# Optimization experiments

Hardware: AMD Instinct MI355X
Metric: run time of the kernel (lower is better)

The kernel has to match this reference:

```python
import jax, jax.numpy as jnp
import numpy as np
import math

N_HEAD = 16


def _causal_attn(q, k, v):
    # q: [B,H,L,d], k/v: [B,H,S,d]; standard scaled-dot-product causal attention
    d_k = q.shape[-1]
    s = jnp.einsum('bhqd,bhkd->bhqk', q, k) / math.sqrt(d_k)
    L, S = q.shape[-2], k.shape[-2]
    mask = jnp.tril(jnp.ones((L, S), dtype=bool))
    s = jnp.where(mask, s, -jnp.inf)
    a = jax.nn.softmax(s, axis=-1)
    return jnp.einsum('bhqk,bhkd->bhqd', a, v)


def setup_inputs() -> dict:
    key = jax.random.key(0)
    ks = jax.random.split(key, 8)
    B, T, C = 2, 2048, 1024
    scale = 0.02
    return {
        'x': jax.random.normal(ks[0], (B, T, C), dtype=jnp.float32),
        'W_attn': jax.random.normal(ks[1], (C, 2 * C), dtype=jnp.float32) * scale,
        'b_attn': jnp.zeros((2 * C,), dtype=jnp.float32),
        'W_k2': jax.random.normal(ks[2], (C, C), dtype=jnp.float32) * scale,
        'b_k2': jnp.zeros((C,), dtype=jnp.float32),
        'W_proj': jax.random.normal(ks[3], (C, C), dtype=jnp.float32) * scale,
        'b_proj': jnp.zeros((C,), dtype=jnp.float32),
    }


def reference(x, W_attn, b_attn, W_k2, b_k2, W_proj, b_proj):
    # Eval-mode forward of CausalSelfAttentionARMA (all dropouts inactive).
    B, T, C = x.shape
    H = N_HEAD
    d = C // H

    qk = x @ W_attn + b_attn                      # [B,T,2C]
    q, k = qk[..., :C], qk[..., C:]
    q = q.reshape(B, T, H, d).transpose(0, 2, 1, 3)   # [B,H,T,d]
    k = k.reshape(B, T, H, d).transpose(0, 2, 1, 3)
    v = x.reshape(B, T, H, d).transpose(0, 2, 1, 3)   # v = x (no value proj)

    # AR pass: standard causal attention
    y = _causal_attn(q, k, v)                     # [B,H,T,d]

    # MA residual: e_t = v_{t+1} - y_t
    e = v[:, :, 1:, :] - y[:, :, :-1, :]          # [B,H,T-1,d]

    k2 = (x[:, :-1] @ W_k2 + b_k2).reshape(B, T - 1, H, d).transpose(0, 2, 1, 3)
    q2 = q[:, :, 1:, :]

    # MA pass: second causal attention over residuals
    y2 = _causal_attn(q2, k2, e)                  # [B,H,T-1,d]
    y2 = jnp.concatenate([jnp.zeros_like(y2[:, :, :1, :]), y2], axis=2)  # [B,H,T,d]

    def proj(t):
        return t.transpose(0, 2, 1, 3).reshape(B, T, C) @ W_proj + b_proj

    return proj(y) + proj(y2)
```

## Files before the change

kernel.cpp:

```cpp
#include <hip/hip_runtime.h>
#include <hip/hip_bf16.h>

typedef unsigned short u16;
typedef short s16x8 __attribute__((ext_vector_type(8)));
typedef float f32x4 __attribute__((ext_vector_type(4)));
typedef float f32x16 __attribute__((ext_vector_type(16)));
typedef unsigned int u32x4 __attribute__((ext_vector_type(4)));

#define LOG2E 1.44269504088896f

__device__ __forceinline__ u16 f2b(float f){
    __hip_bfloat16 h = __float2bfloat16(f);
    return __builtin_bit_cast(unsigned short, h);
}
__device__ __forceinline__ float b2f(u16 u){
    __hip_bfloat16 h = __builtin_bit_cast(__hip_bfloat16, u);
    return __bfloat162float(h);
}
__device__ __forceinline__ unsigned int pk2(float a, float b){
    return (unsigned int)f2b(a) | ((unsigned int)f2b(b) << 16);
}

__global__ void k_f32_to_bf16(const float* __restrict__ in, u16* __restrict__ out, int n4){
    int i = blockIdx.x*blockDim.x + threadIdx.x;
    int stride = gridDim.x*blockDim.x;
    for (; i < n4; i += stride){
        float4 a = *(const float4*)&in[(size_t)i*4];
        uint2 o;
        o.x = pk2(a.x, a.y);
        o.y = pk2(a.z, a.w);
        *(uint2*)&out[(size_t)i*4] = o;
    }
}

__global__ void k_transpose_bf16(const float* __restrict__ W, u16* __restrict__ Wt, int K, int N){
    __shared__ float tile[32][33];
    int n0 = blockIdx.x*32, k0 = blockIdx.y*32;
    int c = threadIdx.x & 31, r0 = threadIdx.x >> 5;
#pragma unroll
    for (int it = 0; it < 4; ++it){
        int r = r0 + it*8;
        tile[r][c] = W[(size_t)(k0+r)*N + n0 + c];
    }
    __syncthreads();
#pragma unroll
    for (int it = 0; it < 4; ++it){
        int r = r0 + it*8;
        Wt[(size_t)(n0+r)*K + k0 + c] = f2b(tile[c][r]);
    }
}

__global__ __launch_bounds__(256) void k_build_vT(const float* __restrict__ x, u16* __restrict__ VT){
    __shared__ float tile[64][65];
    int bh = blockIdx.x, t0 = blockIdx.y*64;
    int b = bh >> 4, h = bh & 15;
    int tid = threadIdx.x;
    {
        int tt = tid >> 2, ds = (tid & 3)*16;
        const float* xp = &x[((size_t)(b*2048) + t0 + tt)*1024 + h*64 + ds];
#pragma unroll
        for (int j4 = 0; j4 < 4; ++j4){
            float4 a = *(const float4*)&xp[j4*4];
            tile[tt][ds + j4*4 + 0] = a.x;
            tile[tt][ds + j4*4 + 1] = a.y;
            tile[tt][ds + j4*4 + 2] = a.z;
            tile[tt][ds + j4*4 + 3] = a.w;
        }
    }
    __syncthreads();
    {
        int dd = tid >> 2, ts = (tid & 3)*16;
        unsigned int o[8];
#pragma unroll
        for (int j = 0; j < 8; ++j)
            o[j] = pk2(tile[ts + 2*j][dd], tile[ts + 2*j + 1][dd]);
        u16* dst = &VT[((size_t)(bh*64 + dd))*2048 + t0 + ts];
        *(uint4*)&dst[0] = *(uint4*)&o[0];
        *(uint4*)&dst[8] = *(uint4*)&o[4];
    }
}

__global__ __launch_bounds__(256) void k_compute_eT(const float* __restrict__ x, const float* __restrict__ y1T,
                                                    u16* __restrict__ ET){
    __shared__ float tile[64][65];
    int bh = blockIdx.x, j0 = blockIdx.y*64;
    int b = bh >> 4, h = bh & 15;
    int tid = threadIdx.x;
    {
        int tt = tid >> 2, ds = (tid & 3)*16;
        int j = j0 + tt;
        int xr = (j <= 2046) ? (j + 1) : 2047;
        const float* xp = &x[((size_t)(b*2048) + xr)*1024 + h*64 + ds];
#pragma unroll
        for (int j4 = 0; j4 < 4; ++j4){
            float4 a = *(const float4*)&xp[j4*4];
            tile[tt][ds + j4*4 + 0] = a.x;
            tile[tt][ds + j4*4 + 1] = a.y;
            tile[tt][ds + j4*4 + 2] = a.z;
            tile[tt][ds + j4*4 + 3] = a.w;
        }
    }
    __syncthreads();
    {
        int dd = tid >> 2, ts = (tid & 3)*16;
        const float* yp = &y1T[((size_t)(bh*64 + dd))*2048 + j0 + ts];
        unsigned int o[8];
#pragma unroll
        for (int j = 0; j < 8; ++j){
            int c0 = ts + 2*j, c1 = ts + 2*j + 1;
            float e0 = (j0 + c0 <= 2046) ? (tile[c0][dd] - yp[2*j])   : 0.f;
            float e1 = (j0 + c1 <= 2046) ? (tile[c1][dd] - yp[2*j+1]) : 0.f;
            o[j] = pk2(e0, e1);
        }
        u16* dst = &ET[((size_t)(bh*64 + dd))*2048 + j0 + ts];
        *(uint4*)&dst[0] = *(uint4*)&o[0];
        *(uint4*)&dst[8] = *(uint4*)&o[4];
    }
}

template<int MODE>
__global__ __launch_bounds__(256) void k_gemm(const u16* __restrict__ A, const u16* __restrict__ Bt,
                       const float* __restrict__ bias, float* __restrict__ outF,
                       u16* __restrict__ out0, u16* __restrict__ out1,
                       int M, int N, int K){
    __shared__ u16 As[128][72];
    __shared__ u16 Bs[128][72];
    int m0 = blockIdx.y * 128, n0 = blockIdx.x * 128;
    int tid = threadIdx.x;
    int lane = tid & 63, w = tid >> 6;
    int wm = w >> 1, wn = w & 1;
    int l15 = lane & 15, l4 = lane >> 4;
    f32x4 acc[4][4] = {};

    for (int kt = 0; kt < K; kt += 64){
#pragma unroll
        for (int it = 0; it < 4; ++it){
            int c = tid + 256*it;
            int row = c >> 3, seg = c & 7;
            *(uint4*)&As[row][seg*8] = *(const uint4*)&A[(size_t)(m0+row)*K + kt + seg*8];
            *(uint4*)&Bs[row][seg*8] = *(const uint4*)&Bt[(size_t)(n0+row)*K + kt + seg*8];
        }
        __syncthreads();
#pragma unroll
        for (int kk = 0; kk < 2; ++kk){
            s16x8 a[4], b[4];
#pragma unroll
            for (int mi = 0; mi < 4; ++mi)
                a[mi] = *(const s16x8*)&As[wm*64 + mi*16 + l15][kk*32 + l4*8];
#pragma unroll
            for (int ni = 0; ni < 4; ++ni)
                b[ni] = *(const s16x8*)&Bs[wn*64 + ni*16 + l15][kk*32 + l4*8];
#pragma unroll
            for (int mi = 0; mi < 4; ++mi)
#pragma unroll
                for (int ni = 0; ni < 4; ++ni)
                    acc[mi][ni] = __builtin_amdgcn_mfma_f32_16x16x32_bf16(a[mi], b[ni], acc[mi][ni], 0,0,0);
        }
        __syncthreads();
    }

#pragma unroll
    for (int mi = 0; mi < 4; ++mi){
        int growb = m0 + wm*64 + mi*16 + l4*4;
#pragma unroll
        for (int ni = 0; ni < 4; ++ni){
            int gcol = n0 + wn*64 + ni*16 + l15;
            float bv = bias[gcol];
#pragma unroll
            for (int r = 0; r < 4; ++r){
                int row = growb + r;
                float val = acc[mi][ni][r];
                if (MODE == 2){
                    outF[(size_t)row*N + gcol] = val + 2.0f*bv;
                } else {
                    val += bv;
                    int bb = row >> 11, t = row & 2047;
                    if (MODE == 0){
                        if (gcol < 1024){
                            int h = gcol >> 6, dd = gcol & 63;
                            out0[(((size_t)(bb*16+h))*2048 + t)*64 + dd] = f2b(val*0.125f);
                        } else {
                            int c2 = gcol - 1024;
                            int h = c2 >> 6, dd = c2 & 63;
                            out1[(((size_t)(bb*16+h))*2048 + t)*64 + dd] = f2b(val);
                        }
                    } else {
                        int h = gcol >> 6, dd = gcol & 63;
                        out0[(((size_t)(bb*16+h))*2048 + t)*64 + dd] = f2b(val);
                    }
                }
            }
        }
    }
}

__global__ __launch_bounds__(256) void k_flash32(const u16* __restrict__ Q, const u16* __restrict__ Km,
                         const u16* __restrict__ VT, float* __restrict__ OT,
                         int Tq, int Tkv, int qoff){
    __shared__ u16 Ks[64*64];
    __shared__ u16 Vs[64*64];
    int bh = blockIdx.x;
    int yy = blockIdx.y;
    int t = (yy < 8) ? yy : (15 - (yy - 8));
    int tid = threadIdx.x;
    int lane = tid & 63, w = tid >> 6;
    int l31 = lane & 31, hi = lane >> 5;
    const u16* Qp = Q + ((size_t)bh*2048 + qoff)*64;
    const u16* Kp = Km + (size_t)bh*2048*64;
    const u16* Vp = VT + (size_t)bh*64*2048;
    float* Op = OT + (size_t)bh*64*2048;

    int srow = tid >> 2;
    int sc   = tid & 3;

    int ntile = 2*t + 2;
    int q0w = t*128 + w*32;
    int qi = q0w + l31; if (qi > Tq-1) qi = Tq-1;

    s16x8 qf[4];
#pragma unroll
    for (int st = 0; st < 4; ++st)
        qf[st] = *(const s16x8*)&Qp[(size_t)qi*64 + st*16 + hi*8];

    f32x16 accO[2] = {};
    float m_r = -INFINITY, l_r = 0.f;

    uint4 kr0, kr1, vr0, vr1;
    {
        int kvr = srow; if (kvr > Tkv-1) kvr = Tkv-1;
        kr0 = *(const uint4*)&Kp[(size_t)kvr*64 + sc*16];
        kr1 = *(const uint4*)&Kp[(size_t)kvr*64 + sc*16 + 8];
        vr0 = *(const uint4*)&Vp[(size_t)srow*2048 + sc*16];
        vr1 = *(const uint4*)&Vp[(size_t)srow*2048 + sc*16 + 8];
    }

    for (int i = 0; i < ntile; ++i){
        int kv0 = i*64;
        {
            int sw = srow & 7;
            *(uint4*)&Ks[srow*64 + (((2*sc)   ^ sw)*8)] = kr0;
            *(uint4*)&Ks[srow*64 + (((2*sc+1) ^ sw)*8)] = kr1;
            *(uint4*)&Vs[srow*64 + (((2*sc)   ^ sw)*8)] = vr0;
            *(uint4*)&Vs[srow*64 + (((2*sc+1) ^ sw)*8)] = vr1;
        }
        __syncthreads();
        if (i + 1 < ntile){
            int kv1 = kv0 + 64;
            int kvr = kv1 + srow; if (kvr > Tkv-1) kvr = Tkv-1;
            kr0 = *(const uint4*)&Kp[(size_t)kvr*64 + sc*16];
            kr1 = *(const uint4*)&Kp[(size_t)kvr*64 + sc*16 + 8];
            vr0 = *(const uint4*)&Vp[(size_t)srow*2048 + kv1 + sc*16];
            vr1 = *(const uint4*)&Vp[(size_t)srow*2048 + kv1 + sc*16 + 8];
        }
        if (kv0 <= q0w + 31){
            f32x16 accS[2] = {};
            __builtin_amdgcn_s_setprio(1);
#pragma unroll
            for (int m = 0; m < 2; ++m){
                int row = 32*m + l31;
                int sw = row & 7;
#pragma unroll
                for (int st = 0; st < 4; ++st){
                    s16x8 a = *(const s16x8*)&Ks[row*64 + (((2*st + hi) ^ sw)*8)];
                    accS[m] = __builtin_amdgcn_mfma_f32_32x32x16_bf16(a, qf[st], accS[m], 0,0,0);
                }
            }
            __builtin_amdgcn_s_setprio(0);
            float p[32];
            bool diag = (kv0 + 63 > q0w);
#pragma unroll
            for (int m = 0; m < 2; ++m)
#pragma unroll
                for (int r = 0; r < 16; ++r){
                    float s = accS[m][r];
                    if (diag){
                        int kg = kv0 + 32*m + (r&3) + 8*(r>>2) + 4*hi;
                        if (kg > qi) s = -INFINITY;
                    }
                    p[m*16 + r] = s;
                }
            float mx = p[0];
#pragma unroll
            for (int j = 1; j < 32; ++j) mx = fmaxf(mx, p[j]);
            mx = fmaxf(mx, __shfl_xor(mx, 32));
            float mnew = fmaxf(m_r, mx);
            if (!__all(mx - m_r <= 8.f)){
                float scl = exp2f((m_r - mnew)*LOG2E);
#pragma unroll
                for (int dt = 0; dt < 2; ++dt)
#pragma unroll
                    for (int r = 0; r < 16; ++r) accO[dt][r] *= scl;
                l_r *= scl;
                m_r = mnew;
            }
            float rs = 0.f;
#pragma unroll
            for (int j = 0; j < 32; ++j){
                p[j] = exp2f((p[j] - m_r)*LOG2E);
                rs += p[j];
            }
            rs += __shfl_xor(rs, 32);
            l_r += rs;
#pragma unroll
            for (int m = 0; m < 2; ++m)
#pragma unroll
                for (int s2 = 0; s2 < 2; ++s2){
                    const float* pp = &p[m*16 + s2*8];
                    unsigned dwa = pk2(pp[0], pp[1]);
                    unsigned dwb = pk2(pp[2], pp[3]);
                    unsigned dwc = pk2(pp[4], pp[5]);
                    unsigned dwd = pk2(pp[6], pp[7]);
                    unsigned xa = (unsigned)__shfl_xor((int)dwa, 32);
                    unsigned xb = (unsigned)__shfl_xor((int)dwb, 32);
                    unsigned xc = (unsigned)__shfl_xor((int)dwc, 32);
                    unsigned xd = (unsigned)__shfl_xor((int)dwd, 32);
                    u32x4 fv;
                    fv.x = hi ? xc : dwa;
                    fv.y = hi ? xd : dwb;
                    fv.z = hi ? dwc : xa;
                    fv.w = hi ? dwd : xb;
                    s16x8 pf = __builtin_bit_cast(s16x8, fv);
                    int vslot = m*4 + s2*2 + hi;
                    __builtin_amdgcn_s_setprio(1);
#pragma unroll
                    for (int dt = 0; dt < 2; ++dt){
                        int vrow = dt*32 + l31;
                        s16x8 va = *(const s16x8*)&Vs[vrow*64 + ((vslot ^ (vrow&7))*8)];
                        accO[dt] = __builtin_amdgcn_mfma_f32_32x32x16_bf16(va, pf, accO[dt], 0,0,0);
                    }
                    __builtin_amdgcn_s_setprio(0);
                }
        }
        __syncthreads();
    }
    float inv = 1.0f / l_r;
#pragma unroll
    for (int dt = 0; dt < 2; ++dt)
#pragma unroll
        for (int r = 0; r < 16; ++r){
            int d = dt*32 + (r&3) + 8*(r>>2) + 4*hi;
            Op[(size_t)d*2048 + qi] = accO[dt][r] * inv;
        }
}

__global__ __launch_bounds__(256) void k_ysum(const float* __restrict__ y1T, const float* __restrict__ y2T,
                                              u16* __restrict__ ys){
    __shared__ float tile[64][65];
    int bh = blockIdx.x, t0 = blockIdx.y*64;
    int b = bh >> 4, h = bh & 15;
    int tid = threadIdx.x;
    {
        int dd = tid >> 2, ts = (tid & 3)*16;
        const float* y1p = &y1T[((size_t)(bh*64 + dd))*2048 + t0 + ts];
        const float* y2p = &y2T[((size_t)(bh*64 + dd))*2048 + t0 + ts - 1];
#pragma unroll
        for (int c = 0; c < 16; ++c){
            int tg = t0 + ts + c;
            float s = y1p[c];
            if (tg > 0) s += y2p[c];
            tile[ts + c][dd] = s;
        }
    }
    __syncthreads();
    {
        int tt = tid >> 2, ds = (tid & 3)*16;
        unsigned int o[8];
#pragma unroll
        for (int j = 0; j < 8; ++j)
            o[j] = pk2(tile[tt][ds + 2*j], tile[tt][ds + 2*j + 1]);
        u16* dst = &ys[((size_t)(b*2048) + t0 + tt)*1024 + h*64 + ds];
        *(uint4*)&dst[0] = *(uint4*)&o[0];
        *(uint4*)&dst[8] = *(uint4*)&o[4];
    }
}

extern "C" void kernel_launch(void* const* d_in, const int* in_sizes, int n_in,
                              void* d_out, int out_size, void* d_ws, size_t ws_size,
                              hipStream_t stream){
    const float* x      = (const float*)d_in[0];
    const float* W_attn = (const float*)d_in[1];
    const float* b_attn = (const float*)d_in[2];
    const float* W_k2   = (const float*)d_in[3];
    const float* b_k2   = (const float*)d_in[4];
    const float* W_proj = (const float*)d_in[5];
    const float* b_proj = (const float*)d_in[6];
    float* out = (float*)d_out;

    char* ws = (char*)d_ws;
    size_t off = 0;
    auto alloc = [&](size_t bytes)->void*{
        void* p = ws + off; off += (bytes + 255) & ~size_t(255); return p;
    };
    u16* xb    = (u16*)alloc((size_t)4096*1024*2);
    u16* WaT   = (u16*)alloc((size_t)2048*1024*2);
    u16* Wk2T  = (u16*)alloc((size_t)1024*1024*2);
    u16* WpT   = (u16*)alloc((size_t)1024*1024*2);
    u16* Qb    = (u16*)alloc((size_t)32*2048*64*2);
    u16* Kb    = (u16*)alloc((size_t)32*2048*64*2);
    u16* VTg   = (u16*)alloc((size_t)32*64*2048*2);
    u16* K2b   = (u16*)alloc((size_t)32*2048*64*2);
    u16* ETg   = (u16*)alloc((size_t)32*64*2048*2);
    float* y1T = (float*)alloc((size_t)32*64*2048*4);
    float* y2T = (float*)alloc((size_t)32*64*2048*4);
    u16* ys    = (u16*)alloc((size_t)4096*1024*2);

    k_f32_to_bf16<<<1024, 256, 0, stream>>>(x, xb, 1<<20);
    k_transpose_bf16<<<dim3(64, 32), 256, 0, stream>>>(W_attn, WaT, 1024, 2048);
    k_transpose_bf16<<<dim3(32, 32), 256, 0, stream>>>(W_k2, Wk2T, 1024, 1024);
    k_transpose_bf16<<<dim3(32, 32), 256, 0, stream>>>(W_proj, WpT, 1024, 1024);
    k_build_vT<<<dim3(32, 32), 256, 0, stream>>>(x, VTg);

    k_gemm<0><<<dim3(16, 32), 256, 0, stream>>>(xb, WaT, b_attn, nullptr, Qb, Kb, 4096, 2048, 1024);
    k_gemm<1><<<dim3(8, 32), 256, 0, stream>>>(xb, Wk2T, b_k2, nullptr, K2b, nullptr, 4096, 1024, 1024);

    k_flash32<<<dim3(32, 16), 256, 0, stream>>>(Qb, Kb, VTg, y1T, 2048, 2048, 0);
    k_compute_eT<<<dim3(32, 32), 256, 0, stream>>>(x, y1T, ETg);
    k_flash32<<<dim3(32, 16), 256, 0, stream>>>(Qb, K2b, ETg, y2T, 2047, 2047, 1);
    k_ysum<<<dim3(32, 32), 256, 0, stream>>>(y1T, y2T, ys);

    k_gemm<2><<<dim3(8, 32), 256, 0, stream>>>(ys, WpT, b_proj, out, nullptr, nullptr, 4096, 1024, 1024);
}
```

Before: 359.8 us.

## Rewrite flash attention to read K/V directly from global memory without LDS

The flash kernel no longer stages K and V tiles through shared memory with block-wide barriers. Each wave now loads its MFMA operands straight from global memory, relying on L1/L2 to serve the reuse. Blocks shrink to 128 threads with twice as many blocks, and each wave skips KV tiles past its own causal limit, so only the last tile needs masking. It also packs bf16 with the hardware cvt_pk instruction and folds the softmax scale into an fma. The trade-off is more global/cache traffic and less data reuse per block.

```diff
diff --git a/kernel.cpp b/kernel.cpp
--- a/kernel.cpp
+++ b/kernel.cpp
@@ -19,6 +19,11 @@
 }
 __device__ __forceinline__ unsigned int pk2(float a, float b){
     return (unsigned int)f2b(a) | ((unsigned int)f2b(b) << 16);
+}
+__device__ __forceinline__ unsigned int cvtpk(float lo, float hi){
+    unsigned int r;
+    asm("v_cvt_pk_bf16_f32 %0, %1, %2" : "=v"(r) : "v"(lo), "v"(hi));
+    return r;
 }
 
 __global__ void k_f32_to_bf16(const float* __restrict__ in, u16* __restrict__ out, int n4){
@@ -194,28 +199,24 @@
     }
 }
 
-__global__ __launch_bounds__(256) void k_flash32(const u16* __restrict__ Q, const u16* __restrict__ Km,
+__global__ __launch_bounds__(128) void k_flashw(const u16* __restrict__ Q, const u16* __restrict__ Km,
                          const u16* __restrict__ VT, float* __restrict__ OT,
-                         int Tq, int Tkv, int qoff){
-    __shared__ u16 Ks[64*64];
-    __shared__ u16 Vs[64*64];
+                         int Tq, int qoff){
     int bh = blockIdx.x;
-    int yy = blockIdx.y;
-    int t = (yy < 8) ? yy : (15 - (yy - 8));
+    int y = blockIdx.y;
+    int t = (y < 16) ? (15 - (y >> 1)) : ((y - 16) >> 1);
+    int half = y & 1;
     int tid = threadIdx.x;
-    int lane = tid & 63, w = tid >> 6;
+    int w = tid >> 6, lane = tid & 63;
     int l31 = lane & 31, hi = lane >> 5;
     const u16* Qp = Q + ((size_t)bh*2048 + qoff)*64;
     const u16* Kp = Km + (size_t)bh*2048*64;
     const u16* Vp = VT + (size_t)bh*64*2048;
     float* Op = OT + (size_t)bh*64*2048;
 
-    int srow = tid >> 2;
-    int sc   = tid & 3;
-
-    int ntile = 2*t + 2;
-    int q0w = t*128 + w*32;
+    int q0w = t*128 + half*64 + w*32;
     int qi = q0w + l31; if (qi > Tq-1) qi = Tq-1;
+    int nt = (q0w >> 6) + 1;
 
     s16x8 qf[4];
 #pragma unroll
@@ -225,113 +226,103 @@
     f32x16 accO[2] = {};
     float m_r = -INFINITY, l_r = 0.f;
 
-    uint4 kr0, kr1, vr0, vr1;
-    {
-        int kvr = srow; if (kvr > Tkv-1) kvr = Tkv-1;
-        kr0 = *(const uint4*)&Kp[(size_t)kvr*64 + sc*16];
-        kr1 = *(const uint4*)&Kp[(size_t)kvr*64 + sc*16 + 8];
-        vr0 = *(const uint4*)&Vp[(size_t)srow*2048 + sc*16];
-        vr1 = *(const uint4*)&Vp[(size_t)srow*2048 + sc*16 + 8];
-    }
-
-    for (int i = 0; i < ntile; ++i){
+    for (int i = 0; i < nt; ++i){
         int kv0 = i*64;
+        const u16* kb = Kp + (size_t)kv0*64;
+        f32x16 s0 = {}, s1 = {};
         {
-            int sw = srow & 7;
-            *(uint4*)&Ks[srow*64 + (((2*sc)   ^ sw)*8)] = kr0;
-            *(uint4*)&Ks[srow*64 + (((2*sc+1) ^ sw)*8)] = kr1;
-            *(uint4*)&Vs[srow*64 + (((2*sc)   ^ sw)*8)] = vr0;
-            *(uint4*)&Vs[srow*64 + (((2*sc+1) ^ sw)*8)] = vr1;
-        }
-        __syncthreads();
-        if (i + 1 < ntile){
-            int kv1 = kv0 + 64;
-            int kvr = kv1 + srow; if (kvr > Tkv-1) kvr = Tkv-1;
-            kr0 = *(const uint4*)&Kp[(size_t)kvr*64 + sc*16];
-            kr1 = *(const uint4*)&Kp[(size_t)kvr*64 + sc*16 + 8];
-            vr0 = *(const uint4*)&Vp[(size_t)srow*2048 + kv1 + sc*16];
-            vr1 = *(const uint4*)&Vp[(size_t)srow*2048 + kv1 + sc*16 + 8];
-        }
-        if (kv0 <= q0w + 31){
-            f32x16 accS[2] = {};
+            const u16* kr0 = kb + (size_t)l31*64 + hi*8;
+            const u16* kr1 = kb + (size_t)(32 + l31)*64 + hi*8;
+            s16x8 a0 = *(const s16x8*)&kr0[0];
+            s16x8 a1 = *(const s16x8*)&kr0[16];
+            s16x8 a2 = *(const s16x8*)&kr0[32];
+            s16x8 a3 = *(const s16x8*)&kr0[48];
+            s16x8 b0 = *(const s16x8*)&kr1[0];
+            s16x8 b1 = *(const s16x8*)&kr1[16];
+            s16x8 b2 = *(const s16x8*)&kr1[32];
+            s16x8 b3 = *(const s16x8*)&kr1[48];
             __builtin_amdgcn_s_setprio(1);
-#pragma unroll
-            for (int m = 0; m < 2; ++m){
-                int row = 32*m + l31;
-                int sw = row & 7;
-#pragma unroll
-                for (int st = 0; st < 4; ++st){
-                    s16x8 a = *(const s16x8*)&Ks[row*64 + (((2*st + hi) ^ sw)*8)];
-                    accS[m] = __builtin_amdgcn_mfma_f32_32x32x16_bf16(a, qf[st], accS[m], 0,0,0);
-                }
+            s0 = __builtin_amdgcn_mfma_f32_32x32x16_bf16(a0, qf[0], s0, 0,0,0);
+            s1 = __builtin_amdgcn_mfma_f32_32x32x16_bf16(b0, qf[0], s1, 0,0,0);
+            s0 = __builtin_amdgcn_mfma_f32_32x32x16_bf16(a1, qf[1], s0, 0,0,0);
+            s1 = __builtin_amdgcn_mfma_f32_32x32x16_bf16(b1, qf[1], s1, 0,0,0);
+            s0 = __builtin_amdgcn_mfma_f32_32x32x16_bf16(a2, qf[2], s0, 0,0,0);
+            s1 = __builtin_amdgcn_mfma_f32_32x32x16_bf16(b2, qf[2], s1, 0,0,0);
+            s0 = __builtin_amdgcn_mfma_f32_32x32x16_bf16(a3, qf[3], s0, 0,0,0);
+            s1 = __builtin_amdgcn_mfma_f32_32x32x16_bf16(b3, qf[3], s1, 0,0,0);
+            __builtin_amdgcn_s_setprio(0);
+        }
+        if (i == nt - 1){
+#pragma unroll
+            for (int r = 0; r < 16; ++r){
+                int kg0 = kv0 + (r&3) + 8*(r>>2) + 4*hi;
+                if (kg0 > qi) s0[r] = -INFINITY;
+                if (kg0 + 32 > qi) s1[r] = -INFINITY;
             }
+        }
+        float mx = s0[0];
+#pragma unroll
+        for (int r = 1; r < 16; ++r) mx = fmaxf(mx, s0[r]);
+#pragma unroll
+        for (int r = 0; r < 16; ++r) mx = fmaxf(mx, s1[r]);
+        mx = fmaxf(mx, __shfl_xor(mx, 32));
+        float mnew = fmaxf(m_r, mx);
+        if (!__all(mx - m_r <= 8.f)){
+            float scl = exp2f((m_r - mnew)*LOG2E);
+#pragma unroll
+            for (int dt = 0; dt < 2; ++dt)
+#pragma unroll
+                for (int r = 0; r < 16; ++r) accO[dt][r] *= scl;
+            l_r *= scl;
+            m_r = mnew;
+        }
+        float bl = m_r * LOG2E;
+        float rs = 0.f;
+#pragma unroll
+        for (int r = 0; r < 16; ++r){
+            s0[r] = exp2f(__builtin_fmaf(s0[r], LOG2E, -bl));
+            rs += s0[r];
+        }
+#pragma unroll
+        for (int r = 0; r < 16; ++r){
+            s1[r] = exp2f(__builtin_fmaf(s1[r], LOG2E, -bl));
+            rs += s1[r];
+        }
+        rs += __shfl_xor(rs, 32);
+        l_r += rs;
+#pragma unroll
+        for (int g = 0; g < 4; ++g){
+            int off = (g & 1)*8;
+            unsigned dwa, dwb, dwc, dwd;
+            if (g < 2){
+                dwa = cvtpk(s0[off+0], s0[off+1]);
+                dwb = cvtpk(s0[off+2], s0[off+3]);
+                dwc = cvtpk(s0[off+4], s0[off+5]);
+                dwd = cvtpk(s0[off+6], s0[off+7]);
+            } else {
+                dwa = cvtpk(s1[off+0], s1[off+1]);
+                dwb = cvtpk(s1[off+2], s1[off+3]);
+                dwc = cvtpk(s1[off+4], s1[off+5]);
+                dwd = cvtpk(s1[off+6], s1[off+7]);
+            }
+            unsigned xa = (unsigned)__shfl_xor((int)dwa, 32);
+            unsigned xb = (unsigned)__shfl_xor((int)dwb, 32);
+            unsigned xc = (unsigned)__shfl_xor((int)dwc, 32);
+            unsigned xd = (unsigned)__shfl_xor((int)dwd, 32);
+            u32x4 fv;
+            fv.x = hi ? xc : dwa;
+            fv.y = hi ? xd : dwb;
+            fv.z = hi ? dwc : xa;
+            fv.w = hi ? dwd : xb;
+            s16x8 pf = __builtin_bit_cast(s16x8, fv);
+            int vslot = g*2 + hi;
+            s16x8 va0 = *(const s16x8*)&Vp[(size_t)l31*2048 + kv0 + vslot*8];
+            s16x8 va1 = *(const s16x8*)&Vp[(size_t)(32 + l31)*2048 + kv0 + vslot*8];
+            __builtin_amdgcn_s_setprio(1);
+            accO[0] = __builtin_amdgcn_mfma_f32_32x32x16_bf16(va0, pf, accO[0], 0,0,0);
+            accO[1] = __builtin_amdgcn_mfma_f32_32x32x16_bf16(va1, pf, accO[1], 0,0,0);
             __builtin_amdgcn_s_setprio(0);
-            float p[32];
-            bool diag = (kv0 + 63 > q0w);
-#pragma unroll
-            for (int m = 0; m < 2; ++m)
-#pragma unroll
-                for (int r = 0; r < 16; ++r){
-                    float s = accS[m][r];
-                    if (diag){
-                        int kg = kv0 + 32*m + (r&3) + 8*(r>>2) + 4*hi;
-                        if (kg > qi) s = -INFINITY;
-                    }
-                    p[m*16 + r] = s;
-                }
-            float mx = p[0];
-#pragma unroll
-            for (int j = 1; j < 32; ++j) mx = fmaxf(mx, p[j]);
-            mx = fmaxf(mx, __shfl_xor(mx, 32));
-            float mnew = fmaxf(m_r, mx);
-            if (!__all(mx - m_r <= 8.f)){
-                float scl = exp2f((m_r - mnew)*LOG2E);
-#pragma unroll
-                for (int dt = 0; dt < 2; ++dt)
-#pragma unroll
-                    for (int r = 0; r < 16; ++r) accO[dt][r] *= scl;
-                l_r *= scl;
-                m_r = mnew;
-            }
-            float rs = 0.f;
-#pragma unroll
-            for (int j = 0; j < 32; ++j){
-                p[j] = exp2f((p[j] - m_r)*LOG2E);
-                rs += p[j];
-            }
-            rs += __shfl_xor(rs, 32);
-            l_r += rs;
-#pragma unroll
-            for (int m = 0; m < 2; ++m)
-#pragma unroll
-                for (int s2 = 0; s2 < 2; ++s2){
-                    const float* pp = &p[m*16 + s2*8];
-                    unsigned dwa = pk2(pp[0], pp[1]);
-                    unsigned dwb = pk2(pp[2], pp[3]);
-                    unsigned dwc = pk2(pp[4], pp[5]);
-                    unsigned dwd = pk2(pp[6], pp[7]);
-                    unsigned xa = (unsigned)__shfl_xor((int)dwa, 32);
-                    unsigned xb = (unsigned)__shfl_xor((int)dwb, 32);
-                    unsigned xc = (unsigned)__shfl_xor((int)dwc, 32);
-                    unsigned xd = (unsigned)__shfl_xor((int)dwd, 32);
-                    u32x4 fv;
-                    fv.x = hi ? xc : dwa;
-                    fv.y = hi ? xd : dwb;
-                    fv.z = hi ? dwc : xa;
-                    fv.w = hi ? dwd : xb;
-                    s16x8 pf = __builtin_bit_cast(s16x8, fv);
-                    int vslot = m*4 + s2*2 + hi;
-                    __builtin_amdgcn_s_setprio(1);
-#pragma unroll
-                    for (int dt = 0; dt < 2; ++dt){
-                        int vrow = dt*32 + l31;
-                        s16x8 va = *(const s16x8*)&Vs[vrow*64 + ((vslot ^ (vrow&7))*8)];
-                        accO[dt] = __builtin_amdgcn_mfma_f32_32x32x16_bf16(va, pf, accO[dt], 0,0,0);
-                    }
-                    __builtin_amdgcn_s_setprio(0);
-                }
-        }
-        __syncthreads();
+        }
     }
     float inv = 1.0f / l_r;
 #pragma unroll
@@ -413,9 +404,9 @@
     k_gemm<0><<<dim3(16, 32), 256, 0, stream>>>(xb, WaT, b_attn, nullptr, Qb, Kb, 4096, 2048, 1024);
     k_gemm<1><<<dim3(8, 32), 256, 0, stream>>>(xb, Wk2T, b_k2, nullptr, K2b, nullptr, 4096, 1024, 1024);
 
-    k_flash32<<<dim3(32, 16), 256, 0, stream>>>(Qb, Kb, VTg, y1T, 2048, 2048, 0);
+    k_flashw<<<dim3(32, 32), 128, 0, stream>>>(Qb, Kb, VTg, y1T, 2048, 0);
     k_compute_eT<<<dim3(32, 32), 256, 0, stream>>>(x, y1T, ETg);
-    k_flash32<<<dim3(32, 16), 256, 0, stream>>>(Qb, K2b, ETg, y2T, 2047, 2047, 1);
+    k_flashw<<<dim3(32, 32), 128, 0, stream>>>(Qb, K2b, ETg, y2T, 2047, 1);
     k_ysum<<<dim3(32, 32), 256, 0, stream>>>(y1T, y2T, ys);
 
     k_gemm<2><<<dim3(8, 32), 256, 0, stream>>>(ys, WpT, b_proj, out, nullptr, nullptr, 4096, 1024, 1024);
```

New measurement: 363.5 us. About the same (+1.0%).
